# Kernel tuning notes

Measured on AMD Instinct MI355X. Metric: run time of the kernel, lower is better.

Reference implementation:

```python
import jax, jax.numpy as jnp
import numpy as np

B, T, H, L = 64, 64, 256, 2
INPUT_SIZE = 65
E = INPUT_SIZE - 1  # encoder_in


def setup_inputs() -> dict:
    key = jax.random.key(0)
    ks = jax.random.split(key, 20)
    s = 0.05
    p = {}
    p["input_data"] = jax.random.normal(ks[0], (B, T, INPUT_SIZE), jnp.float32)
    # encoder LSTM (input E -> H, L layers; torch gate order i,f,g,o)
    p["w_ih_e0"] = jax.random.normal(ks[1], (4 * H, E), jnp.float32) * s
    p["w_ih_e1"] = jax.random.normal(ks[2], (L - 1, 4 * H, H), jnp.float32) * s
    p["w_hh_e"] = jax.random.normal(ks[3], (L, 4 * H, H), jnp.float32) * s
    p["b_ih_e"] = jax.random.normal(ks[4], (L, 4 * H), jnp.float32) * s
    p["b_hh_e"] = jax.random.normal(ks[5], (L, 4 * H), jnp.float32) * s
    # decoder LSTM (input H+1 -> H, L layers)
    p["w_ih_d0"] = jax.random.normal(ks[6], (4 * H, H + 1), jnp.float32) * s
    p["w_ih_d1"] = jax.random.normal(ks[7], (L - 1, 4 * H, H), jnp.float32) * s
    p["w_hh_d"] = jax.random.normal(ks[8], (L, 4 * H, H), jnp.float32) * s
    p["b_ih_d"] = jax.random.normal(ks[9], (L, 4 * H), jnp.float32) * s
    p["b_hh_d"] = jax.random.normal(ks[10], (L, 4 * H), jnp.float32) * s
    # encoder attention MLP: Linear(2H+T -> E), Tanh, Linear(E -> 1, no bias)
    p["attn_w1"] = jax.random.normal(ks[11], (E, 2 * H + T), jnp.float32) * s
    p["attn_b1"] = jax.random.normal(ks[12], (E,), jnp.float32) * s
    p["attn_w2"] = jax.random.normal(ks[13], (E,), jnp.float32) * s
    # decoder attention MLP: Linear(3H -> H), Tanh, Linear(H -> 1, no bias)
    p["attnd_w1"] = jax.random.normal(ks[14], (H, 3 * H), jnp.float32) * s
    p["attnd_b1"] = jax.random.normal(ks[15], (H,), jnp.float32) * s
    p["attnd_w2"] = jax.random.normal(ks[16], (H,), jnp.float32) * s
    # output projection: Linear(2H -> 1)
    p["proj_w"] = jax.random.normal(ks[17], (1, 2 * H), jnp.float32) * s
    p["proj_b"] = jax.random.normal(ks[18], (1,), jnp.float32) * s
    return p


def _lstm_step(x, h, c, w_ih0, w_ih_rest, w_hh, b_ih, b_hh):
    """Single-timestep multi-layer LSTM. x: [B, in], h/c: [L, B, H]."""
    hs, cs = [], []
    inp = x
    for l in range(L):
        w_ih = w_ih0 if l == 0 else w_ih_rest[l - 1]
        gates = inp @ w_ih.T + b_ih[l] + h[l] @ w_hh[l].T + b_hh[l]  # [B, 4H]
        i, f, g, o = jnp.split(gates, 4, axis=-1)
        c_new = jax.nn.sigmoid(f) * c[l] + jax.nn.sigmoid(i) * jnp.tanh(g)
        h_new = jax.nn.sigmoid(o) * jnp.tanh(c_new)
        hs.append(h_new)
        cs.append(c_new)
        inp = h_new
    return jnp.stack(hs), jnp.stack(cs)


def reference(input_data, w_ih_e0, w_ih_e1, w_hh_e, b_ih_e, b_hh_e,
              w_ih_d0, w_ih_d1, w_hh_d, b_ih_d, b_hh_d,
              attn_w1, attn_b1, attn_w2, attnd_w1, attnd_b1, attnd_w2,
              proj_w, proj_b):
    input_encoder = input_data[:, :, 1:]             # [B, T, E]
    input_decoder = input_data[:, :, 0]              # [B, T]
    input_permuted = jnp.transpose(input_encoder, (0, 2, 1))  # [B, E, T]

    h0 = jnp.zeros((L, B, H), input_data.dtype)
    c0 = jnp.zeros((L, B, H), input_data.dtype)

    def enc_step(carry, x_t):  # x_t: [B, E]
        h, c = carry
        feat = jnp.concatenate([
            jnp.broadcast_to(h[-1][:, None, :], (B, E, H)),
            jnp.broadcast_to(c[-1][:, None, :], (B, E, H)),
            input_permuted], axis=-1)                # [B, E, 2H+T]
        z = jnp.tanh(feat @ attn_w1.T + attn_b1)     # [B, E, E]
        a = jax.nn.softmax(z @ attn_w2, axis=-1)     # [B, E]
        h, c = _lstm_step(x_t * a, h, c, w_ih_e0, w_ih_e1, w_hh_e, b_ih_e, b_hh_e)
        return (h, c), h[-1]

    _, h_tops = jax.lax.scan(enc_step, (h0, c0), jnp.transpose(input_encoder, (1, 0, 2)))
    h_expanded = jnp.transpose(h_tops, (1, 0, 2))    # [B, T, H]

    def dec_step(carry, d_t):  # d_t: [B]
        h, c = carry
        feat = jnp.concatenate([
            jnp.broadcast_to(h[-1][:, None, :], (B, T, H)),
            jnp.broadcast_to(c[-1][:, None, :], (B, T, H)),
            h_expanded], axis=-1)                    # [B, T, 3H]
        z = jnp.tanh(feat @ attnd_w1.T + attnd_b1)   # [B, T, H]
        a = jax.nn.softmax(z @ attnd_w2, axis=-1)    # [B, T]
        partial = jnp.einsum('bth,bt->bh', h_expanded, a)  # [B, H]
        full = jnp.concatenate([partial, d_t[:, None]], axis=-1)  # [B, H+1]
        h, c = _lstm_step(full, h, c, w_ih_d0, w_ih_d1, w_hh_d, b_ih_d, b_hh_d)
        return (h, c), partial

    (h_d, c_d), partials = jax.lax.scan(dec_step, (h0, c0), input_decoder.T)
    out = jnp.abs(jnp.concatenate([h_d[-1], partials[-1]], axis=-1) @ proj_w.T + proj_b)  # [B, 1]
    return out
```

## Files before the change

kernel.cpp:

```cpp
#include <hip/hip_runtime.h>
#include <hip/hip_fp16.h>
#include <math.h>

#define NT 1024

typedef _Float16 h2v __attribute__((ext_vector_type(2)));
union H8 { uint4 u; h2v h[4]; };

__device__ __forceinline__ float sigf(float x)   { return 1.0f / (1.0f + __expf(-x)); }
__device__ __forceinline__ float tanhf_(float x) { return 1.0f - 2.0f / (1.0f + __expf(2.0f * x)); }
__device__ __forceinline__ float dot4(float4 a, float4 b) {
    return a.x * b.x + a.y * b.y + a.z * b.z + a.w * b.w;
}
__device__ __forceinline__ float red16(float v) {
    v += __shfl_xor(v, 1); v += __shfl_xor(v, 2);
    v += __shfl_xor(v, 4); v += __shfl_xor(v, 8);
    return v;
}
__device__ __forceinline__ float red64(float v) {
    v += __shfl_xor(v, 1);  v += __shfl_xor(v, 2);  v += __shfl_xor(v, 4);
    v += __shfl_xor(v, 8);  v += __shfl_xor(v, 16); v += __shfl_xor(v, 32);
    return v;
}
__device__ __forceinline__ float dot2h(h2v a, h2v b, float c) {
#if __has_builtin(__builtin_amdgcn_fdot2)
    return __builtin_amdgcn_fdot2(a, b, c, false);
#else
    return c + (float)a[0] * (float)b[0] + (float)a[1] * (float)b[1];
#endif
}

__device__ __forceinline__ float exr(const float* p) {
    return __hip_atomic_load(p, __ATOMIC_RELAXED, __HIP_MEMORY_SCOPE_AGENT);
}

__device__ __forceinline__ void xbar(unsigned* ctr, unsigned target) {
    asm volatile("s_waitcnt vmcnt(0)" ::: "memory");
    __syncthreads();
    if (threadIdx.x == 0) {
        __hip_atomic_fetch_add(ctr, 1u, __ATOMIC_RELAXED, __HIP_MEMORY_SCOPE_AGENT);
        while (__hip_atomic_load(ctr, __ATOMIC_RELAXED, __HIP_MEMORY_SCOPE_AGENT) < target)
            __builtin_amdgcn_s_sleep(1);
    }
    __syncthreads();
}

#define OFF_RA   0
#define OFF_RE0  32768
#define OFF_RE1  425984
#define OFF_RDW1 950272
#define OFF_RD0  1081344
#define OFF_RDT  1605632
#define OFF_RD1  1606656
#define TOT_H    2130944

template<int ITERS, bool BIAS, bool DT>
__device__ __forceinline__ void gemv512x(const __half* __restrict__ W,
                                         const __half* __restrict__ act,
                                         const float* __restrict__ bias,
                                         const __half* __restrict__ rdt, float dts,
                                         float* __restrict__ outg,
                                         int jBase, int ljBase) {
    const int lane = threadIdx.x & 63;
    const int q = lane & 15, g = lane >> 4;
    H8 a0, a1, a2, a3;
    a0.u = *(const uint4*)(act + 8 * q);
    a1.u = *(const uint4*)(act + 8 * q + 128);
    a2.u = *(const uint4*)(act + 8 * q + 256);
    a3.u = *(const uint4*)(act + 8 * q + 384);
    #pragma unroll 2
    for (int it = 0; it < ITERS; ++it) {
        const int j = jBase + it * 4 + g;
        const uint4* wp = (const uint4*)(W + ((size_t)j << 9) + 32 * q);
        H8 w0, w1, w2, w3;
        w0.u = wp[0]; w1.u = wp[1]; w2.u = wp[2]; w3.u = wp[3];
        float s0 = 0.f, s1 = 0.f;
        #pragma unroll
        for (int i = 0; i < 4; ++i) {
            s0 = dot2h(w0.h[i], a0.h[i], s0);
            s1 = dot2h(w1.h[i], a1.h[i], s1);
            s0 = dot2h(w2.h[i], a2.h[i], s0);
            s1 = dot2h(w3.h[i], a3.h[i], s1);
        }
        float s = s0 + s1;
        s += __shfl_xor(s, 1); s += __shfl_xor(s, 2);
        s += __shfl_xor(s, 4); s += __shfl_xor(s, 8);
        if (q == 0) {
            if (DT) s += dts * (float)rdt[j];
            outg[ljBase + it * 4 + g] = BIAS ? s + bias[j] : s;
        }
    }
}

template<int ITERS>
__device__ __forceinline__ void gemv384x(const __half* __restrict__ W,
                                         const __half* __restrict__ act,
                                         const float* __restrict__ bias,
                                         float* __restrict__ outg,
                                         int jBase, int ljBase) {
    const int lane = threadIdx.x & 63;
    const int q = lane & 15, g = lane >> 4;
    H8 a0, a1, a2;
    a0.u = *(const uint4*)(act + 8 * q);
    a1.u = *(const uint4*)(act + 8 * q + 128);
    a2.u = *(const uint4*)(act + 8 * q + 256);
    #pragma unroll 2
    for (int it = 0; it < ITERS; ++it) {
        const int j = jBase + it * 4 + g;
        const uint4* wp = (const uint4*)(W + (size_t)j * 384 + 24 * q);
        H8 w0, w1, w2;
        w0.u = wp[0]; w1.u = wp[1]; w2.u = wp[2];
        float s0 = 0.f, s1 = 0.f;
        #pragma unroll
        for (int i = 0; i < 4; ++i) {
            s0 = dot2h(w0.h[i], a0.h[i], s0);
            s1 = dot2h(w1.h[i], a1.h[i], s1);
            s0 = dot2h(w2.h[i], a2.h[i], s0);
        }
        float s = s0 + s1;
        s += __shfl_xor(s, 1); s += __shfl_xor(s, 2);
        s += __shfl_xor(s, 4); s += __shfl_xor(s, 8);
        if (q == 0) outg[ljBase + it * 4 + g] = s + bias[j];
    }
}

#define M_HEXP  0
#define M_XET   16384
#define M_GSL   20736
#define M_HCT   20992
#define M_TMP   21248
#define M_SCORE 21312
#define M_AS    21376
#define M_C0    21440
#define M_C1    21504
#define M_HC1F  21568
#define M_DECIN 21824
#define M_PARTF 21888
#define M_BE0   22144
#define M_BE1   23168
#define M_BD0   24192
#define M_BD1   25216
#define M_AHC   26240
#define M_AE0   26496
#define M_AHH   26688
#define M_AD0   26944
#define M_RDT   27200
#define M_TOT   27712

extern "C" __global__ void __launch_bounds__(NT)
attn_lstm_v6(const float* __restrict__ inp,  const __half* __restrict__ wsh,
             float* __restrict__ h0x, float* __restrict__ h1x,
             float* __restrict__ hcx, unsigned* __restrict__ barc,
             const float* __restrict__ bihe, const float* __restrict__ bhhe,
             const float* __restrict__ bihd, const float* __restrict__ bhhd,
             const float* __restrict__ aw1,  const float* __restrict__ ab1,
             const float* __restrict__ aw2,
             const float* __restrict__ dw1,  const float* __restrict__ db1,
             const float* __restrict__ dw2,
             const float* __restrict__ pw,   const float* __restrict__ pb,
             float* __restrict__ out)
{
    extern __shared__ __align__(16) float sm[];
    float* hexp   = sm + M_HEXP;
    float* xeT    = sm + M_XET;
    float* gsl    = sm + M_GSL;
    float* hctL   = sm + M_HCT;
    float* tmp64  = sm + M_TMP;
    float* scoreS = sm + M_SCORE;
    float* aS     = sm + M_AS;
    float* c0L    = sm + M_C0;
    float* c1L    = sm + M_C1;
    float* hc1f   = sm + M_HC1F;
    float* decin  = sm + M_DECIN;
    float* partF  = sm + M_PARTF;
    float* bE0    = sm + M_BE0;
    float* bE1    = sm + M_BE1;
    float* bD0    = sm + M_BD0;
    float* bD1    = sm + M_BD1;
    __half* aHC   = (__half*)(sm + M_AHC);
    __half* aE0   = (__half*)(sm + M_AE0);
    __half* aHH   = (__half*)(sm + M_AHH);
    __half* aD0   = (__half*)(sm + M_AD0);
    __half* rdtL  = (__half*)(sm + M_RDT);

    const __half* RA   = wsh + OFF_RA;
    const __half* RE0  = wsh + OFF_RE0;
    const __half* RE1  = wsh + OFF_RE1;
    const __half* RDW1 = wsh + OFF_RDW1;
    const __half* RD0  = wsh + OFF_RD0;
    const __half* RD1  = wsh + OFF_RD1;

    const int tid = threadIdx.x;
    const int b   = blockIdx.x >> 2;
    const int co  = blockIdx.x & 3;
    const int w   = tid >> 6;
    unsigned* ctr = barc + (b << 4);
    unsigned  ph  = 0;

    if (tid < 64) { c0L[tid] = 0.f; c1L[tid] = 0.f; }
    for (int i = tid; i < 960; i += NT) sm[M_AHC + i] = 0.0f;
    if (tid < 512) sm[M_RDT + tid] = ((const float*)(wsh + OFF_RDT))[tid];
    {
        int j = tid;
        bE0[j] = bihe[j]        + bhhe[j];
        bE1[j] = bihe[1024 + j] + bhhe[1024 + j];
        bD0[j] = bihd[j]        + bhhd[j];
        bD1[j] = bihd[1024 + j] + bhhd[1024 + j];
    }
    const float* ib = inp + b * (64 * 65);
    for (int i = tid; i < 4096; i += NT) {
        int t = i & 63, e = i >> 6;
        xeT[e * 68 + t] = ib[t * 65 + 1 + e];
    }
    if (tid < 64) decin[tid] = ib[tid * 65];
    __syncthreads();

    const int g16 = tid >> 4, q16 = tid & 15;
    const int gg = w >> 2, cb = (w & 3) << 4;
    const int jB  = gg * 256 + co * 64 + cb;
    const int ljB = gg * 64 + cb;

    float Preg[4], w2r[4];
    #pragma unroll
    for (int jj = 0; jj < 4; ++jj) {
        int j = q16 + 16 * jj;
        w2r[jj] = aw2[j];
        float acc = ab1[j];
        const float4* w4 = (const float4*)(aw1 + j * 576 + 512);
        const float4* x4 = (const float4*)(xeT + g16 * 68);
        #pragma unroll 4
        for (int k = 0; k < 16; ++k) acc += dot4(w4[k], x4[k]);
        Preg[jj] = acc;
    }

    for (int t = 0; t < 64; ++t) {
        const int p = t & 1;
        float* h0b = h0x + p * 16384 + b * 256;
        float* h1b = h1x + p * 32768 + b * 512;
        gemv512x<1, false, false>(RA, aHC, nullptr, nullptr, 0.f, hctL, w * 4, w * 4);
        __syncthreads();
        {
            float s = 0.f;
            #pragma unroll
            for (int jj = 0; jj < 4; ++jj)
                s += tanhf_(Preg[jj] + hctL[q16 + 16 * jj]) * w2r[jj];
            s = red16(s);
            if (q16 == 0) scoreS[g16] = s;
        }
        __syncthreads();
        if (tid < 64) {
            float v = scoreS[tid], m = v;
            #pragma unroll
            for (int d = 1; d < 64; d <<= 1) m = fmaxf(m, __shfl_xor(m, d));
            float ex = __expf(v - m), s = ex;
            #pragma unroll
            for (int d = 1; d < 64; d <<= 1) s += __shfl_xor(s, d);
            aE0[tid] = __float2half((ex / s) * xeT[tid * 68 + t]);
        }
        __syncthreads();
        gemv384x<4>(RE0, aE0, bE0, gsl, jB, ljB);
        __syncthreads();
        if (tid < 64) {
            float cn = sigf(gsl[64 + tid]) * c0L[tid] + sigf(gsl[tid]) * tanhf_(gsl[128 + tid]);
            float hn = sigf(gsl[192 + tid]) * tanhf_(cn);
            c0L[tid] = cn;
            atomicExch(&h0b[co * 64 + tid], hn);
        }
        xbar(ctr, ++ph * 4u);
        if (tid < 256) {
            __half hh = __float2half(exr(&h0b[tid]));
            aE0[64 + tid] = hh; aHH[tid] = hh;
        }
        __syncthreads();
        gemv512x<4, true, false>(RE1, aHH, bE1, nullptr, 0.f, gsl, jB, ljB);
        __syncthreads();
        if (tid < 64) {
            float cn = sigf(gsl[64 + tid]) * c1L[tid] + sigf(gsl[tid]) * tanhf_(gsl[128 + tid]);
            float hn = sigf(gsl[192 + tid]) * tanhf_(cn);
            c1L[tid] = cn;
            atomicExch(&h1b[co * 64 + tid], hn);
            atomicExch(&h1b[256 + co * 64 + tid], cn);
        }
        xbar(ctr, ++ph * 4u);
        if (tid < 512) {
            float v = exr(&h1b[tid]);
            __half hh = __float2half(v);
            aHC[tid] = hh;
            if (tid < 256) { aHH[256 + tid] = hh; hexp[t * 256 + tid] = v; }
        }
        __syncthreads();
    }

    if (tid < 64) { c0L[tid] = 0.f; c1L[tid] = 0.f; }
    for (int i = tid; i < 960; i += NT) sm[M_AHC + i] = 0.0f;
    __syncthreads();
    float Pdreg[16], w2dr[16];
    #pragma unroll
    for (int jj = 0; jj < 16; ++jj) {
        int j = q16 + 16 * jj;
        w2dr[jj] = dw2[j];
        float acc = db1[j];
        const float4* w4 = (const float4*)(dw1 + j * 768 + 512);
        const float4* x4 = (const float4*)(hexp + g16 * 256);
        #pragma unroll 4
        for (int k = 0; k < 64; ++k) acc += dot4(w4[k], x4[k]);
        Pdreg[jj] = acc;
    }
    __syncthreads();

    const int j4 = tid >> 2, q4 = tid & 3;
    for (int t = 0; t < 64; ++t) {
        const int p = t & 1;
        float* h0b = h0x + p * 16384 + b * 256;
        float* h1b = h1x + p * 32768 + b * 512;
        float* hcb = hcx + p * 16384 + b * 256;
        gemv512x<1, false, false>(RDW1, aHC, nullptr, nullptr, 0.f, tmp64,
                                  co * 64 + w * 4, w * 4);
        __syncthreads();
        if (tid < 64) atomicExch(&hcb[co * 64 + tid], tmp64[tid]);
        xbar(ctr, ++ph * 4u);
        if (tid < 256) hctL[tid] = exr(&hcb[tid]);
        __syncthreads();
        {
            float s = 0.f;
            #pragma unroll
            for (int jj = 0; jj < 16; ++jj)
                s += tanhf_(Pdreg[jj] + hctL[q16 + 16 * jj]) * w2dr[jj];
            s = red16(s);
            if (q16 == 0) scoreS[g16] = s;
        }
        __syncthreads();
        if (tid < 64) {
            float v = scoreS[tid], m = v;
            #pragma unroll
            for (int d = 1; d < 64; d <<= 1) m = fmaxf(m, __shfl_xor(m, d));
            float ex = __expf(v - m), s = ex;
            #pragma unroll
            for (int d = 1; d < 64; d <<= 1) s += __shfl_xor(s, d);
            aS[tid] = ex / s;
        }
        __syncthreads();
        {
            float acc = 0.f;
            #pragma unroll 4
            for (int i = 0; i < 16; ++i) {
                int tt = q4 + 4 * i;
                acc += hexp[tt * 256 + j4] * aS[tt];
            }
            acc += __shfl_xor(acc, 1);
            acc += __shfl_xor(acc, 2);
            if (q4 == 0) { aD0[j4] = __float2half(acc); partF[j4] = acc; }
        }
        __syncthreads();
        gemv512x<4, true, true>(RD0, aD0, bD0, rdtL, decin[t], gsl, jB, ljB);
        __syncthreads();
        if (tid < 64) {
            float cn = sigf(gsl[64 + tid]) * c0L[tid] + sigf(gsl[tid]) * tanhf_(gsl[128 + tid]);
            float hn = sigf(gsl[192 + tid]) * tanhf_(cn);
            c0L[tid] = cn;
            atomicExch(&h0b[co * 64 + tid], hn);
        }
        xbar(ctr, ++ph * 4u);
        if (tid < 256) {
            __half hh = __float2half(exr(&h0b[tid]));
            aD0[256 + tid] = hh; aHH[tid] = hh;
        }
        __syncthreads();
        gemv512x<4, true, false>(RD1, aHH, bD1, nullptr, 0.f, gsl, jB, ljB);
        __syncthreads();
        if (tid < 64) {
            float cn = sigf(gsl[64 + tid]) * c1L[tid] + sigf(gsl[tid]) * tanhf_(gsl[128 + tid]);
            float hn = sigf(gsl[192 + tid]) * tanhf_(cn);
            c1L[tid] = cn;
            atomicExch(&h1b[co * 64 + tid], hn);
            atomicExch(&h1b[256 + co * 64 + tid], cn);
        }
        xbar(ctr, ++ph * 4u);
        if (tid < 512) {
            float v = exr(&h1b[tid]);
            __half hh = __float2half(v);
            aHC[tid] = hh;
            if (tid < 256) { aHH[256 + tid] = hh; hc1f[tid] = v; }
        }
        __syncthreads();
    }

    if (co == 0 && tid < 64) {
        float acc = 0.f;
        #pragma unroll
        for (int i = 0; i < 8; ++i) {
            int k = tid + 64 * i;
            float v = (k < 256) ? hc1f[k] : partF[k - 256];
            acc += v * pw[k];
        }
        acc = red64(acc);
        if (tid == 0) out[b] = fabsf(acc + pb[0]);
    }
}

#define L_HEXP   0
#define L_XET    16384
#define L_GSL    20736
#define L_HCT    21760
#define L_SCORE  22016
#define L_AS     22080
#define L_C0     22144
#define L_HC1F   22400
#define L_DECIN  22912
#define L_PARTF  22976
#define L_BE0    23232
#define L_BE1    24256
#define L_BD0    25280
#define L_BD1    26304
#define L_AHC    27328
#define L_AE0    27584
#define L_AHH    27776
#define L_AD0    28032
#define L_RDT    28288
#define L_TOT    28800

extern "C" __global__ void __launch_bounds__(NT)
attn_lstm_v5(const float* __restrict__ inp,  const __half* __restrict__ wsh,
             const float* __restrict__ bihe, const float* __restrict__ bhhe,
             const float* __restrict__ bihd, const float* __restrict__ bhhd,
             const float* __restrict__ aw1,  const float* __restrict__ ab1,
             const float* __restrict__ aw2,
             const float* __restrict__ dw1,  const float* __restrict__ db1,
             const float* __restrict__ dw2,
             const float* __restrict__ pw,   const float* __restrict__ pb,
             float* __restrict__ out)
{
    extern __shared__ __align__(16) float sm[];
    float* hexp   = sm + L_HEXP;
    float* xeT    = sm + L_XET;
    float* gsl    = sm + L_GSL;
    float* hctL   = sm + L_HCT;
    float* scoreS = sm + L_SCORE;
    float* aS     = sm + L_AS;
    float* c0L    = sm + L_C0;
    float* hc1f   = sm + L_HC1F;
    float* decin  = sm + L_DECIN;
    float* partF  = sm + L_PARTF;
    float* bE0    = sm + L_BE0;
    float* bE1    = sm + L_BE1;
    float* bD0    = sm + L_BD0;
    float* bD1    = sm + L_BD1;
    __half* aHC   = (__half*)(sm + L_AHC);
    __half* aE0   = (__half*)(sm + L_AE0);
    __half* aHH   = (__half*)(sm + L_AHH);
    __half* aD0   = (__half*)(sm + L_AD0);
    __half* rdtL  = (__half*)(sm + L_RDT);

    const __half* RA   = wsh + OFF_RA;
    const __half* RE0  = wsh + OFF_RE0;
    const __half* RE1  = wsh + OFF_RE1;
    const __half* RDW1 = wsh + OFF_RDW1;
    const __half* RD0  = wsh + OFF_RD0;
    const __half* RD1  = wsh + OFF_RD1;

    const int b   = blockIdx.x;
    const int tid = threadIdx.x;
    const int w   = tid >> 6;

    for (int i = tid; i < (L_BE0 - L_C0); i += NT) sm[L_C0 + i] = 0.0f;
    for (int i = tid; i < (L_RDT - L_AHC); i += NT) sm[L_AHC + i] = 0.0f;
    if (tid < 512) sm[L_RDT + tid] = ((const float*)(wsh + OFF_RDT))[tid];
    {
        int j = tid;
        bE0[j] = bihe[j]        + bhhe[j];
        bE1[j] = bihe[1024 + j] + bhhe[1024 + j];
        bD0[j] = bihd[j]        + bhhd[j];
        bD1[j] = bihd[1024 + j] + bhhd[1024 + j];
    }
    const float* ib = inp + b * (64 * 65);
    for (int i = tid; i < 4096; i += NT) {
        int t = i & 63, e = i >> 6;
        xeT[e * 68 + t] = ib[t * 65 + 1 + e];
    }
    if (tid < 64) decin[tid] = ib[tid * 65];
    __syncthreads();

    const int g16 = tid >> 4, q16 = tid & 15;

    float Preg[4], w2r[4];
    #pragma unroll
    for (int jj = 0; jj < 4; ++jj) {
        int j = q16 + 16 * jj;
        w2r[jj] = aw2[j];
        float acc = ab1[j];
        const float4* w4 = (const float4*)(aw1 + j * 576 + 512);
        const float4* x4 = (const float4*)(xeT + g16 * 68);
        #pragma unroll 4
        for (int k = 0; k < 16; ++k) acc += dot4(w4[k], x4[k]);
        Preg[jj] = acc;
    }

    for (int t = 0; t < 64; ++t) {
        gemv512x<1, false, false>(RA, aHC, nullptr, nullptr, 0.f, hctL, w * 4, w * 4);
        __syncthreads();
        {
            float s = 0.f;
            #pragma unroll
            for (int jj = 0; jj < 4; ++jj)
                s += tanhf_(Preg[jj] + hctL[q16 + 16 * jj]) * w2r[jj];
            s = red16(s);
            if (q16 == 0) scoreS[g16] = s;
        }
        __syncthreads();
        if (tid < 64) {
            float v = scoreS[tid], m = v;
            #pragma unroll
            for (int d = 1; d < 64; d <<= 1) m = fmaxf(m, __shfl_xor(m, d));
            float ex = __expf(v - m), s = ex;
            #pragma unroll
            for (int d = 1; d < 64; d <<= 1) s += __shfl_xor(s, d);
            aE0[tid] = __float2half((ex / s) * xeT[tid * 68 + t]);
        }
        __syncthreads();
        gemv384x<16>(RE0, aE0, bE0, gsl, w * 64, w * 64);
        __syncthreads();
        if (tid < 256) {
            float cn = sigf(gsl[256 + tid]) * c0L[tid] + sigf(gsl[tid]) * tanhf_(gsl[512 + tid]);
            float hn = sigf(gsl[768 + tid]) * tanhf_(cn);
            c0L[tid] = cn;
            __half hh = __float2half(hn);
            aE0[64 + tid] = hh; aHH[tid] = hh;
        }
        __syncthreads();
        gemv512x<16, true, false>(RE1, aHH, bE1, nullptr, 0.f, gsl, w * 64, w * 64);
        __syncthreads();
        if (tid < 256) {
            float cp = hc1f[256 + tid];
            float cn = sigf(gsl[256 + tid]) * cp + sigf(gsl[tid]) * tanhf_(gsl[512 + tid]);
            float hn = sigf(gsl[768 + tid]) * tanhf_(cn);
            hc1f[tid] = hn; hc1f[256 + tid] = cn;
            __half hh = __float2half(hn);
            aHC[tid] = hh; aHC[256 + tid] = __float2half(cn);
            aHH[256 + tid] = hh;
            hexp[t * 256 + tid] = hn;
        }
        __syncthreads();
    }

    if (tid < 256) { c0L[tid] = 0.0f; hc1f[tid] = 0.0f; hc1f[256 + tid] = 0.0f; }
    for (int i = tid; i < (L_RDT - L_AHC); i += NT) sm[L_AHC + i] = 0.0f;
    __syncthreads();
    float Pdreg[16], w2dr[16];
    #pragma unroll
    for (int jj = 0; jj < 16; ++jj) {
        int j = q16 + 16 * jj;
        w2dr[jj] = dw2[j];
        float acc = db1[j];
        const float4* w4 = (const float4*)(dw1 + j * 768 + 512);
        const float4* x4 = (const float4*)(hexp + g16 * 256);
        #pragma unroll 4
        for (int k = 0; k < 64; ++k) acc += dot4(w4[k], x4[k]);
        Pdreg[jj] = acc;
    }
    __syncthreads();

    const int j4 = tid >> 2, q4 = tid & 3;
    for (int t = 0; t < 64; ++t) {
        gemv512x<4, false, false>(RDW1, aHC, nullptr, nullptr, 0.f, hctL, w * 16, w * 16);
        __syncthreads();
        {
            float s = 0.f;
            #pragma unroll
            for (int jj = 0; jj < 16; ++jj)
                s += tanhf_(Pdreg[jj] + hctL[q16 + 16 * jj]) * w2dr[jj];
            s = red16(s);
            if (q16 == 0) scoreS[g16] = s;
        }
        __syncthreads();
        if (tid < 64) {
            float v = scoreS[tid], m = v;
            #pragma unroll
            for (int d = 1; d < 64; d <<= 1) m = fmaxf(m, __shfl_xor(m, d));
            float ex = __expf(v - m), s = ex;
            #pragma unroll
            for (int d = 1; d < 64; d <<= 1) s += __shfl_xor(s, d);
            aS[tid] = ex / s;
        }
        __syncthreads();
        {
            float acc = 0.f;
            #pragma unroll 4
            for (int i = 0; i < 16; ++i) {
                int tt = q4 + 4 * i;
                acc += hexp[tt * 256 + j4] * aS[tt];
            }
            acc += __shfl_xor(acc, 1);
            acc += __shfl_xor(acc, 2);
            if (q4 == 0) { aD0[j4] = __float2half(acc); partF[j4] = acc; }
        }
        __syncthreads();
        gemv512x<16, true, true>(RD0, aD0, bD0, rdtL, decin[t], gsl, w * 64, w * 64);
        __syncthreads();
        if (tid < 256) {
            float cn = sigf(gsl[256 + tid]) * c0L[tid] + sigf(gsl[tid]) * tanhf_(gsl[512 + tid]);
            float hn = sigf(gsl[768 + tid]) * tanhf_(cn);
            c0L[tid] = cn;
            __half hh = __float2half(hn);
            aD0[256 + tid] = hh; aHH[tid] = hh;
        }
        __syncthreads();
        gemv512x<16, true, false>(RD1, aHH, bD1, nullptr, 0.f, gsl, w * 64, w * 64);
        __syncthreads();
        if (tid < 256) {
            float cp = hc1f[256 + tid];
            float cn = sigf(gsl[256 + tid]) * cp + sigf(gsl[tid]) * tanhf_(gsl[512 + tid]);
            float hn = sigf(gsl[768 + tid]) * tanhf_(cn);
            hc1f[tid] = hn; hc1f[256 + tid] = cn;
            __half hh = __float2half(hn);
            aHC[tid] = hh; aHC[256 + tid] = __float2half(cn);
            aHH[256 + tid] = hh;
        }
        __syncthreads();
    }

    if (tid < 64) {
        float acc = 0.f;
        #pragma unroll
        for (int i = 0; i < 8; ++i) {
            int k = tid + 64 * i;
            float v = (k < 256) ? hc1f[k] : partF[k - 256];
            acc += v * pw[k];
        }
        acc = red64(acc);
        if (tid == 0) out[b] = fabsf(acc + pb[0]);
    }
}

extern "C" __global__ void repack16b(const float* __restrict__ wihe0,
                                     const float* __restrict__ wihe1,
                                     const float* __restrict__ whhe,
                                     const float* __restrict__ wihd0,
                                     const float* __restrict__ wihd1,
                                     const float* __restrict__ whhd,
                                     const float* __restrict__ aw1,
                                     const float* __restrict__ dw1,
                                     __half* __restrict__ ws) {
    int idx = blockIdx.x * blockDim.x + threadIdx.x;
    if (idx >= TOT_H) return;
    int o = idx; float v;
    if (o < 32768) {
        int j = o >> 9, p = o & 511;
        int q = p >> 5, r = p & 31, c = r >> 3, e = r & 7;
        int k = 8 * q + 128 * c + e;
        v = aw1[j * 576 + k];
        ws[OFF_RA + o] = __float2half_rn(v); return;
    }
    o -= 32768;
    if (o < 393216) {
        int j = o / 384, p = o - j * 384;
        int q = p / 24, r = p - q * 24, c = r >> 3, e = r & 7;
        int k = 8 * q + 128 * c + e;
        v = (k < 64) ? wihe0[j * 64 + k] : (k < 320 ? whhe[j * 256 + (k - 64)] : 0.0f);
        ws[OFF_RE0 + o] = __float2half_rn(v); return;
    }
    o -= 393216;
    if (o < 524288) {
        int j = o >> 9, p = o & 511;
        int q = p >> 5, r = p & 31, c = r >> 3, e = r & 7;
        int k = 8 * q + 128 * c + e;
        v = (k < 256) ? wihe1[j * 256 + k] : whhe[262144 + j * 256 + (k - 256)];
        ws[OFF_RE1 + o] = __float2half_rn(v); return;
    }
    o -= 524288;
    if (o < 131072) {
        int j = o >> 9, p = o & 511;
        int q = p >> 5, r = p & 31, c = r >> 3, e = r & 7;
        int k = 8 * q + 128 * c + e;
        v = dw1[j * 768 + k];
        ws[OFF_RDW1 + o] = __float2half_rn(v); return;
    }
    o -= 131072;
    if (o < 524288) {
        int j = o >> 9, p = o & 511;
        int q = p >> 5, r = p & 31, c = r >> 3, e = r & 7;
        int k = 8 * q + 128 * c + e;
        v = (k < 256) ? wihd0[j * 257 + k] : whhd[j * 256 + (k - 256)];
        ws[OFF_RD0 + o] = __float2half_rn(v); return;
    }
    o -= 524288;
    if (o < 1024) {
        v = wihd0[o * 257 + 256];
        ws[OFF_RDT + o] = __float2half_rn(v); return;
    }
    o -= 1024;
    {
        int j = o >> 9, p = o & 511;
        int q = p >> 5, r = p & 31, c = r >> 3, e = r & 7;
        int k = 8 * q + 128 * c + e;
        v = (k < 256) ? wihd1[j * 256 + k] : whhd[262144 + j * 256 + (k - 256)];
        ws[OFF_RD1 + o] = __float2half_rn(v);
    }
}

extern "C" void kernel_launch(void* const* d_in, const int* in_sizes, int n_in,
                              void* d_out, int out_size, void* d_ws, size_t ws_size,
                              hipStream_t stream) {
    const float* inp   = (const float*)d_in[0];
    const float* wihe0 = (const float*)d_in[1];
    const float* wihe1 = (const float*)d_in[2];
    const float* whhe  = (const float*)d_in[3];
    const float* bihe  = (const float*)d_in[4];
    const float* bhhe  = (const float*)d_in[5];
    const float* wihd0 = (const float*)d_in[6];
    const float* wihd1 = (const float*)d_in[7];
    const float* whhd  = (const float*)d_in[8];
    const float* bihd  = (const float*)d_in[9];
    const float* bhhd  = (const float*)d_in[10];
    const float* aw1   = (const float*)d_in[11];
    const float* ab1   = (const float*)d_in[12];
    const float* aw2   = (const float*)d_in[13];
    const float* dw1   = (const float*)d_in[14];
    const float* db1   = (const float*)d_in[15];
    const float* dw2   = (const float*)d_in[16];
    const float* pw    = (const float*)d_in[17];
    const float* pb    = (const float*)d_in[18];
    float* out = (float*)d_out;

    const size_t EX0 = TOT_H / 2;
    const size_t H0X = EX0;
    const size_t H1X = EX0 + 32768;
    const size_t HCX = EX0 + 98304;
    const size_t CTR = EX0 + 131072;
    const size_t NEED6 = (CTR + 1024) * sizeof(float);

    if (ws_size >= NEED6) {
        float* ws32 = (float*)d_ws;
        __half* wsh = (__half*)d_ws;
        hipMemsetAsync((char*)d_ws + CTR * sizeof(float), 0, 4096, stream);
        repack16b<<<(TOT_H + 255) / 256, 256, 0, stream>>>(
            wihe0, wihe1, whhe, wihd0, wihd1, whhd, aw1, dw1, wsh);
        const int smem = M_TOT * 4;
        hipFuncSetAttribute((const void*)attn_lstm_v6,
                            hipFuncAttributeMaxDynamicSharedMemorySize, smem);
        attn_lstm_v6<<<256, NT, smem, stream>>>(
            inp, wsh, ws32 + H0X, ws32 + H1X, ws32 + HCX,
            (unsigned*)(ws32 + CTR),
            bihe, bhhe, bihd, bhhd,
            aw1, ab1, aw2, dw1, db1, dw2, pw, pb, out);
        return;
    }

    if (ws_size >= (size_t)TOT_H * sizeof(__half)) {
        __half* wsh = (__half*)d_ws;
        repack16b<<<(TOT_H + 255) / 256, 256, 0, stream>>>(
            wihe0, wihe1, whhe, wihd0, wihd1, whhd, aw1, dw1, wsh);
        const int smem = L_TOT * 4;
        hipFuncSetAttribute((const void*)attn_lstm_v5,
                            hipFuncAttributeMaxDynamicSharedMemorySize, smem);
        attn_lstm_v5<<<64, NT, smem, stream>>>(
            inp, wsh, bihe, bhhe, bihd, bhhd,
            aw1, ab1, aw2, dw1, db1, dw2, pw, pb, out);
    }
}
```

Measured before the change: 2.253 ms.

## Split grid barrier into signal/wait, prefetch weights into registers, drop decoder hc barrier

The grid barrier is split into a signal and a wait, and the next stage's weight rows are loaded into registers between them, so weight fetch latency overlaps the cross-block wait. The decoder now computes the full hc projection redundantly in each block instead of splitting it across blocks, which removes one grid barrier and one global exchange per decoder step. The cost is more register pressure from the prefetch buffers and duplicated GEMV work for the RDW1 projection.

```diff
diff --git a/kernel.cpp b/kernel.cpp
--- a/kernel.cpp
+++ b/kernel.cpp
@@ -34,11 +34,14 @@
     return __hip_atomic_load(p, __ATOMIC_RELAXED, __HIP_MEMORY_SCOPE_AGENT);
 }
 
-__device__ __forceinline__ void xbar(unsigned* ctr, unsigned target) {
-    asm volatile("s_waitcnt vmcnt(0)" ::: "memory");
-    __syncthreads();
+__device__ __forceinline__ void xsig(unsigned* ctr) {
     if (threadIdx.x == 0) {
+        asm volatile("s_waitcnt vmcnt(0)" ::: "memory");
         __hip_atomic_fetch_add(ctr, 1u, __ATOMIC_RELAXED, __HIP_MEMORY_SCOPE_AGENT);
+    }
+}
+__device__ __forceinline__ void xwait(unsigned* ctr, unsigned target) {
+    if (threadIdx.x == 0) {
         while (__hip_atomic_load(ctr, __ATOMIC_RELAXED, __HIP_MEMORY_SCOPE_AGENT) < target)
             __builtin_amdgcn_s_sleep(1);
     }
@@ -54,8 +57,9 @@
 #define OFF_RD1  1606656
 #define TOT_H    2130944
 
-template<int ITERS, bool BIAS, bool DT>
-__device__ __forceinline__ void gemv512x(const __half* __restrict__ W,
+template<int ITERS, int PF, bool BIAS, bool DT>
+__device__ __forceinline__ void gemv512p(const __half* __restrict__ W,
+                                         const uint4* __restrict__ pre,
                                          const __half* __restrict__ act,
                                          const float* __restrict__ bias,
                                          const __half* __restrict__ rdt, float dts,
@@ -68,12 +72,17 @@
     a1.u = *(const uint4*)(act + 8 * q + 128);
     a2.u = *(const uint4*)(act + 8 * q + 256);
     a3.u = *(const uint4*)(act + 8 * q + 384);
-    #pragma unroll 2
+    #pragma unroll
     for (int it = 0; it < ITERS; ++it) {
         const int j = jBase + it * 4 + g;
-        const uint4* wp = (const uint4*)(W + ((size_t)j << 9) + 32 * q);
         H8 w0, w1, w2, w3;
-        w0.u = wp[0]; w1.u = wp[1]; w2.u = wp[2]; w3.u = wp[3];
+        if (it < PF) {
+            w0.u = pre[it * 4 + 0]; w1.u = pre[it * 4 + 1];
+            w2.u = pre[it * 4 + 2]; w3.u = pre[it * 4 + 3];
+        } else {
+            const uint4* wp = (const uint4*)(W + ((size_t)j << 9) + 32 * q);
+            w0.u = wp[0]; w1.u = wp[1]; w2.u = wp[2]; w3.u = wp[3];
+        }
         float s0 = 0.f, s1 = 0.f;
         #pragma unroll
         for (int i = 0; i < 4; ++i) {
@@ -89,6 +98,20 @@
             if (DT) s += dts * (float)rdt[j];
             outg[ljBase + it * 4 + g] = BIAS ? s + bias[j] : s;
         }
+    }
+}
+
+template<int PF>
+__device__ __forceinline__ void pf512(const __half* __restrict__ W, int jBase,
+                                      uint4* pre) {
+    const int lane = threadIdx.x & 63;
+    const int q = lane & 15, g = lane >> 4;
+    #pragma unroll
+    for (int it = 0; it < PF; ++it) {
+        const int j = jBase + it * 4 + g;
+        const uint4* wp = (const uint4*)(W + ((size_t)j << 9) + 32 * q);
+        pre[it * 4 + 0] = wp[0]; pre[it * 4 + 1] = wp[1];
+        pre[it * 4 + 2] = wp[2]; pre[it * 4 + 3] = wp[3];
     }
 }
 
@@ -128,7 +151,6 @@
 #define M_XET   16384
 #define M_GSL   20736
 #define M_HCT   20992
-#define M_TMP   21248
 #define M_SCORE 21312
 #define M_AS    21376
 #define M_C0    21440
@@ -148,9 +170,9 @@
 #define M_TOT   27712
 
 extern "C" __global__ void __launch_bounds__(NT)
-attn_lstm_v6(const float* __restrict__ inp,  const __half* __restrict__ wsh,
+attn_lstm_v7(const float* __restrict__ inp,  const __half* __restrict__ wsh,
              float* __restrict__ h0x, float* __restrict__ h1x,
-             float* __restrict__ hcx, unsigned* __restrict__ barc,
+             unsigned* __restrict__ barc,
              const float* __restrict__ bihe, const float* __restrict__ bhhe,
              const float* __restrict__ bihd, const float* __restrict__ bhhd,
              const float* __restrict__ aw1,  const float* __restrict__ ab1,
@@ -165,7 +187,6 @@
     float* xeT    = sm + M_XET;
     float* gsl    = sm + M_GSL;
     float* hctL   = sm + M_HCT;
-    float* tmp64  = sm + M_TMP;
     float* scoreS = sm + M_SCORE;
     float* aS     = sm + M_AS;
     float* c0L    = sm + M_C0;
@@ -233,11 +254,17 @@
         Preg[jj] = acc;
     }
 
+    uint4 preA[4];
+    uint4 preW[8];
+    uint4 preD[8];
+
+    pf512<1>(RA, w * 4, preA);
     for (int t = 0; t < 64; ++t) {
         const int p = t & 1;
         float* h0b = h0x + p * 16384 + b * 256;
         float* h1b = h1x + p * 32768 + b * 512;
-        gemv512x<1, false, false>(RA, aHC, nullptr, nullptr, 0.f, hctL, w * 4, w * 4);
+        gemv512p<1, 1, false, false>(RA, preA, aHC, nullptr, nullptr, 0.f,
+                                     hctL, w * 4, w * 4);
         __syncthreads();
         {
             float s = 0.f;
@@ -266,13 +293,16 @@
             c0L[tid] = cn;
             atomicExch(&h0b[co * 64 + tid], hn);
         }
-        xbar(ctr, ++ph * 4u);
+        xsig(ctr); ++ph;
+        pf512<2>(RE1, jB, preW);
+        xwait(ctr, ph * 4u);
         if (tid < 256) {
             __half hh = __float2half(exr(&h0b[tid]));
             aE0[64 + tid] = hh; aHH[tid] = hh;
         }
         __syncthreads();
-        gemv512x<4, true, false>(RE1, aHH, bE1, nullptr, 0.f, gsl, jB, ljB);
+        gemv512p<4, 2, true, false>(RE1, preW, aHH, bE1, nullptr, 0.f,
+                                    gsl, jB, ljB);
         __syncthreads();
         if (tid < 64) {
             float cn = sigf(gsl[64 + tid]) * c1L[tid] + sigf(gsl[tid]) * tanhf_(gsl[128 + tid]);
@@ -281,7 +311,9 @@
             atomicExch(&h1b[co * 64 + tid], hn);
             atomicExch(&h1b[256 + co * 64 + tid], cn);
         }
-        xbar(ctr, ++ph * 4u);
+        xsig(ctr); ++ph;
+        pf512<1>(RA, w * 4, preA);
+        xwait(ctr, ph * 4u);
         if (tid < 512) {
             float v = exr(&h1b[tid]);
             __half hh = __float2half(v);
@@ -309,17 +341,13 @@
     __syncthreads();
 
     const int j4 = tid >> 2, q4 = tid & 3;
+    pf512<2>(RDW1, w * 16, preD);
     for (int t = 0; t < 64; ++t) {
         const int p = t & 1;
         float* h0b = h0x + p * 16384 + b * 256;
         float* h1b = h1x + p * 32768 + b * 512;
-        float* hcb = hcx + p * 16384 + b * 256;
-        gemv512x<1, false, false>(RDW1, aHC, nullptr, nullptr, 0.f, tmp64,
-                                  co * 64 + w * 4, w * 4);
-        __syncthreads();
-        if (tid < 64) atomicExch(&hcb[co * 64 + tid], tmp64[tid]);
-        xbar(ctr, ++ph * 4u);
-        if (tid < 256) hctL[tid] = exr(&hcb[tid]);
+        gemv512p<4, 2, false, false>(RDW1, preD, aHC, nullptr, nullptr, 0.f,
+                                     hctL, w * 16, w * 16);
         __syncthreads();
         {
             float s = 0.f;
@@ -352,7 +380,8 @@
             if (q4 == 0) { aD0[j4] = __float2half(acc); partF[j4] = acc; }
         }
         __syncthreads();
-        gemv512x<4, true, true>(RD0, aD0, bD0, rdtL, decin[t], gsl, jB, ljB);
+        gemv512p<4, 0, true, true>(RD0, nullptr, aD0, bD0, rdtL, decin[t],
+                                   gsl, jB, ljB);
         __syncthreads();
         if (tid < 64) {
             float cn = sigf(gsl[64 + tid]) * c0L[tid] + sigf(gsl[tid]) * tanhf_(gsl[128 + tid]);
@@ -360,13 +389,16 @@
             c0L[tid] = cn;
             atomicExch(&h0b[co * 64 + tid], hn);
         }
-        xbar(ctr, ++ph * 4u);
+        xsig(ctr); ++ph;
+        pf512<2>(RD1, jB, preW);
+        xwait(ctr, ph * 4u);
         if (tid < 256) {
             __half hh = __float2half(exr(&h0b[tid]));
             aD0[256 + tid] = hh; aHH[tid] = hh;
         }
         __syncthreads();
-        gemv512x<4, true, false>(RD1, aHH, bD1, nullptr, 0.f, gsl, jB, ljB);
+        gemv512p<4, 2, true, false>(RD1, preW, aHH, bD1, nullptr, 0.f,
+                                    gsl, jB, ljB);
         __syncthreads();
         if (tid < 64) {
             float cn = sigf(gsl[64 + tid]) * c1L[tid] + sigf(gsl[tid]) * tanhf_(gsl[128 + tid]);
@@ -375,7 +407,9 @@
             atomicExch(&h1b[co * 64 + tid], hn);
             atomicExch(&h1b[256 + co * 64 + tid], cn);
         }
-        xbar(ctr, ++ph * 4u);
+        xsig(ctr); ++ph;
+        pf512<2>(RDW1, w * 16, preD);
+        xwait(ctr, ph * 4u);
         if (tid < 512) {
             float v = exr(&h1b[tid]);
             __half hh = __float2half(v);
@@ -496,7 +530,7 @@
     }
 
     for (int t = 0; t < 64; ++t) {
-        gemv512x<1, false, false>(RA, aHC, nullptr, nullptr, 0.f, hctL, w * 4, w * 4);
+        gemv512p<1, 0, false, false>(RA, nullptr, aHC, nullptr, nullptr, 0.f, hctL, w * 4, w * 4);
         __syncthreads();
         {
             float s = 0.f;
@@ -527,7 +561,7 @@
             aE0[64 + tid] = hh; aHH[tid] = hh;
         }
         __syncthreads();
-        gemv512x<16, true, false>(RE1, aHH, bE1, nullptr, 0.f, gsl, w * 64, w * 64);
+        gemv512p<16, 0, true, false>(RE1, nullptr, aHH, bE1, nullptr, 0.f, gsl, w * 64, w * 64);
         __syncthreads();
         if (tid < 256) {
             float cp = hc1f[256 + tid];
@@ -561,7 +595,7 @@
 
     const int j4 = tid >> 2, q4 = tid & 3;
     for (int t = 0; t < 64; ++t) {
-        gemv512x<4, false, false>(RDW1, aHC, nullptr, nullptr, 0.f, hctL, w * 16, w * 16);
+        gemv512p<4, 0, false, false>(RDW1, nullptr, aHC, nullptr, nullptr, 0.f, hctL, w * 16, w * 16);
         __syncthreads();
         {
             float s = 0.f;
@@ -594,7 +628,7 @@
             if (q4 == 0) { aD0[j4] = __float2half(acc); partF[j4] = acc; }
         }
         __syncthreads();
-        gemv512x<16, true, true>(RD0, aD0, bD0, rdtL, decin[t], gsl, w * 64, w * 64);
+        gemv512p<16, 0, true, true>(RD0, nullptr, aD0, bD0, rdtL, decin[t], gsl, w * 64, w * 64);
         __syncthreads();
         if (tid < 256) {
             float cn = sigf(gsl[256 + tid]) * c0L[tid] + sigf(gsl[tid]) * tanhf_(gsl[512 + tid]);
@@ -604,7 +638,7 @@
             aD0[256 + tid] = hh; aHH[tid] = hh;
         }
         __syncthreads();
-        gemv512x<16, true, false>(RD1, aHH, bD1, nullptr, 0.f, gsl, w * 64, w * 64);
+        gemv512p<16, 0, true, false>(RD1, nullptr, aHH, bD1, nullptr, 0.f, gsl, w * 64, w * 64);
         __syncthreads();
         if (tid < 256) {
             float cp = hc1f[256 + tid];
@@ -724,21 +758,20 @@
     const size_t EX0 = TOT_H / 2;
     const size_t H0X = EX0;
     const size_t H1X = EX0 + 32768;
-    const size_t HCX = EX0 + 98304;
     const size_t CTR = EX0 + 131072;
-    const size_t NEED6 = (CTR + 1024) * sizeof(float);
-
-    if (ws_size >= NEED6) {
+    const size_t NEED7 = (CTR + 1024) * sizeof(float);
+
+    if (ws_size >= NEED7) {
         float* ws32 = (float*)d_ws;
         __half* wsh = (__half*)d_ws;
         hipMemsetAsync((char*)d_ws + CTR * sizeof(float), 0, 4096, stream);
         repack16b<<<(TOT_H + 255) / 256, 256, 0, stream>>>(
             wihe0, wihe1, whhe, wihd0, wihd1, whhd, aw1, dw1, wsh);
         const int smem = M_TOT * 4;
-        hipFuncSetAttribute((const void*)attn_lstm_v6,
+        hipFuncSetAttribute((const void*)attn_lstm_v7,
                             hipFuncAttributeMaxDynamicSharedMemorySize, smem);
-        attn_lstm_v6<<<256, NT, smem, stream>>>(
-            inp, wsh, ws32 + H0X, ws32 + H1X, ws32 + HCX,
+        attn_lstm_v7<<<256, NT, smem, stream>>>(
+            inp, wsh, ws32 + H0X, ws32 + H1X,
             (unsigned*)(ws32 + CTR),
             bihe, bhhe, bihd, bhhd,
             aw1, ab1, aw2, dw1, db1, dw2, pw, pb, out);
```

Result: slower. 3.669 ms (+62.9%).
